# Kernel tuning notes

Measured on AMD Instinct MI355X. Metric: run time of the kernel, lower is better.

## Reference

```python
import jax, jax.numpy as jnp
import numpy as np


def _rot_mat(thetas, scales):
    # thetas, scales: [bs, g] -> [bs, g, 9, 9] bilinear-interpolation matrices
    bs, g = thetas.shape
    t = thetas.reshape(-1)
    s = scales.reshape(-1)
    x = jnp.cos(t) * s
    y = jnp.sin(t) * s
    yp = -y
    z = jnp.zeros_like(x)
    o = jnp.ones_like(x)
    a = x - y; b = x * y; c = x + y; d = a * c; e = a + c
    ap = x - yp; bp = x * yp; cp = x + yp; dp = ap * cp; ep = ap + cp

    def M(rows):
        # rows: 9 lists of 9 [N]-arrays -> [9, 9, N]
        return jnp.stack([jnp.stack(r, axis=0) for r in rows], axis=0)

    ctr = [z, z, z, z, o, z, z, z, z]

    pb1 = M([
        [a, 1 - a, z, z, z, z, z, z, z],
        [z, 1 - y, y, z, z, z, z, z, z],
        [z, z, a, z, z, 1 - a, z, z, z],
        [y, z, z, 1 - y, z, z, z, z, z],
        ctr,
        [z, z, z, z, z, 1 - y, z, z, y],
        [z, z, z, 1 - a, z, z, a, z, z],
        [z, z, z, z, z, z, y, 1 - y, z],
        [z, z, z, z, z, z, z, 1 - a, a]])
    pb2 = M([
        [a, 1 - a, z, z, z, z, z, z, z],
        [z, x - b, b, z, 1 - c + b, y - b, z, z, z],
        [z, z, a, z, z, 1 - a, z, z, z],
        [b, y - b, z, x - b, 1 - c + b, z, z, z, z],
        ctr,
        [z, z, z, z, 1 - c + b, x - b, z, y - b, b],
        [z, z, z, 1 - a, z, z, a, z, z],
        [z, z, z, y - b, 1 - c + b, z, b, x - b, z],
        [z, z, z, z, z, z, z, 1 - a, a]])
    ps1 = M([
        [d, a - d, z, c - d, 1 - e + d, z, z, z, z],
        [z, x - b, b, z, 1 - c + b, y - b, z, z, z],
        [z, c - d, d, z, 1 - e + d, a - d, z, z, z],
        [b, y - b, z, x - b, 1 - c + b, z, z, z, z],
        ctr,
        [z, z, z, z, 1 - c + b, x - b, z, y - b, b],
        [z, z, z, a - d, 1 - e + d, z, d, c - d, z],
        [z, z, z, y - b, 1 - c + b, z, b, x - b, z],
        [z, z, z, z, 1 - e + d, c - d, z, a - d, d]])
    ps2 = pb2  # identical in the source
    nb1 = M([
        [cp, z, z, 1 - cp, z, z, z, z, z],
        [yp, 1 - yp, z, z, z, z, z, z, z],
        [z, 1 - cp, cp, z, z, z, z, z, z],
        [z, z, z, 1 - yp, z, z, yp, z, z],
        ctr,
        [z, z, yp, z, z, 1 - yp, z, z, z],
        [z, z, z, z, z, z, cp, 1 - cp, z],
        [z, z, z, z, z, z, z, 1 - yp, yp],
        [z, z, z, z, z, 1 - cp, z, z, cp]])
    nb2 = M([
        [cp, z, z, 1 - cp, z, z, z, z, z],
        [bp, x - bp, z, yp - bp, 1 - cp + bp, z, z, z, z],
        [z, 1 - cp, cp, z, z, z, z, z, z],
        [z, z, z, x - bp, 1 - cp + bp, z, bp, yp - bp, z],
        ctr,
        [z, yp - bp, bp, z, 1 - cp + bp, x - bp, z, z, z],
        [z, z, z, z, z, z, cp, 1 - cp, z],
        [z, z, z, z, 1 - cp + bp, yp - bp, z, x - bp, bp],
        [z, z, z, z, z, 1 - cp, z, z, cp]])
    ns1 = M([
        [dp, cp - dp, z, ap - dp, 1 - ep + dp, z, z, z, z],
        [bp, x - bp, z, yp - bp, 1 - cp + bp, z, z, z, z],
        [z, ap - dp, dp, z, 1 - ep + dp, cp - dp, z, z, z],
        [z, yp - bp, bp, z, 1 - cp + bp, x - bp, z, z, z],
        ctr,
        [z, z, z, x - bp, 1 - cp + bp, z, bp, yp - bp, z],
        [z, z, z, cp - dp, 1 - ep + dp, z, dp, ap - dp, z],
        [z, z, z, z, 1 - cp + bp, yp - bp, z, x - bp, bp],
        [z, z, z, z, 1 - ep + dp, ap - dp, z, cp - dp, dp]])
    ns2 = nb2  # mirrors the positive branch where small_2 == big_2

    m_pos = (t >= 0.0)[None, None, :]
    m_big = (s >= 1.0)[None, None, :]
    m_1 = (jnp.abs(t) <= jnp.pi / 4)[None, None, :]
    pos = jnp.where(m_big, jnp.where(m_1, pb1, pb2), jnp.where(m_1, ps1, ps2))
    neg = jnp.where(m_big, jnp.where(m_1, nb1, nb2), jnp.where(m_1, ns1, ns2))
    rot = jnp.where(m_pos, pos, neg)  # [9, 9, bs*g]
    return jnp.transpose(rot, (2, 0, 1)).reshape(bs, g, 9, 9)


def _forward(x, thetas, scales, lambdas, weight):
    # x: [B, Cin, H, W]; weight: [n, Cout, Cin, 3, 3]; thetas/scales/lambdas: [B, n]
    B, Cin, H, W = x.shape
    n, Cout = weight.shape[0], weight.shape[1]
    rot = _rot_mat(thetas, scales) * lambdas[:, :, None, None]  # [B, n, 9, 9]
    w9 = weight.reshape(n, Cout, Cin, 9)
    # per-sample transformed kernel: sum over kernel_number n and source taps j
    w = jnp.einsum('bnij,nocj->bioc', rot, w9)  # [B, 9, Cout, Cin]
    w = jnp.transpose(w, (0, 2, 3, 1)).reshape(B * Cout, Cin, 3, 3)
    xg = x.reshape(1, B * Cin, H, W)
    out = jax.lax.conv_general_dilated(
        xg, w, window_strides=(1, 1), padding=((1, 1), (1, 1)),
        dimension_numbers=('NCHW', 'OIHW', 'NCHW'), feature_group_count=B)
    return out.reshape(B, Cout, H, W)


def setup_inputs() -> dict:
    key = jax.random.key(0)
    ks = jax.random.split(key, 5)
    B, Cin, Cout, H, W, n = 16, 256, 256, 64, 64, 4
    x = jax.random.normal(ks[0], (B, Cin, H, W), dtype=jnp.float32)
    thetas = jax.random.uniform(ks[1], (B, n), minval=-1.2, maxval=1.2, dtype=jnp.float32)
    scales = jax.random.uniform(ks[2], (B, n), minval=0.5, maxval=1.5, dtype=jnp.float32)
    lambdas = jax.nn.softmax(jax.random.normal(ks[3], (B, n), dtype=jnp.float32), axis=-1)
    weight = jax.random.normal(ks[4], (n, Cout, Cin, 3, 3), dtype=jnp.float32) * 0.05
    return {"x": x, "thetas": thetas, "scales": scales, "lambdas": lambdas, "weight": weight}


def reference(x, thetas, scales, lambdas, weight):
    return _forward(x, thetas, scales, lambdas, weight)
```

## Files before the change

### kernel.cpp

```cpp
#include <hip/hip_runtime.h>
#include <cstdint>
#include <cstddef>

typedef unsigned short ushort_t;
typedef __attribute__((ext_vector_type(4))) float f32x4;
typedef __attribute__((ext_vector_type(8))) short s16x8;

#define PI_4F 0.78539816339744830962f

__device__ inline ushort_t f2bf(float f) {
  unsigned int u = __float_as_uint(f);
  u = u + 0x7fffu + ((u >> 16) & 1u);
  return (ushort_t)(u >> 16);
}

__global__ void rot_kernel(const float* __restrict__ thetas, const float* __restrict__ scales,
                           const float* __restrict__ lambdas, float* __restrict__ rot) {
  int tid = threadIdx.x;
  float t = thetas[tid], s = scales[tid], lam = lambdas[tid];
  float xv = cosf(t) * s, yv = sinf(t) * s;
  bool pos = (t >= 0.0f), big = (s >= 1.0f), m1 = (fabsf(t) <= PI_4F);
  float M[81];
#pragma unroll
  for (int i = 0; i < 81; ++i) M[i] = 0.0f;
  M[36 + 4] = 1.0f;
  if (pos) {
    float a = xv - yv, bb = xv * yv, c = xv + yv;
    if (m1 && big) {
      M[0] = a; M[1] = 1 - a;
      M[9 + 1] = 1 - yv; M[9 + 2] = yv;
      M[18 + 2] = a; M[18 + 5] = 1 - a;
      M[27 + 0] = yv; M[27 + 3] = 1 - yv;
      M[45 + 5] = 1 - yv; M[45 + 8] = yv;
      M[54 + 3] = 1 - a; M[54 + 6] = a;
      M[63 + 6] = yv; M[63 + 7] = 1 - yv;
      M[72 + 7] = 1 - a; M[72 + 8] = a;
    } else if (m1) {
      float d = a * c, e = a + c;
      M[0] = d; M[1] = a - d; M[3] = c - d; M[4] = 1 - e + d;
      M[9 + 1] = xv - bb; M[9 + 2] = bb; M[9 + 4] = 1 - c + bb; M[9 + 5] = yv - bb;
      M[18 + 1] = c - d; M[18 + 2] = d; M[18 + 4] = 1 - e + d; M[18 + 5] = a - d;
      M[27 + 0] = bb; M[27 + 1] = yv - bb; M[27 + 3] = xv - bb; M[27 + 4] = 1 - c + bb;
      M[45 + 4] = 1 - c + bb; M[45 + 5] = xv - bb; M[45 + 7] = yv - bb; M[45 + 8] = bb;
      M[54 + 3] = a - d; M[54 + 4] = 1 - e + d; M[54 + 6] = d; M[54 + 7] = c - d;
      M[63 + 3] = yv - bb; M[63 + 4] = 1 - c + bb; M[63 + 6] = bb; M[63 + 7] = xv - bb;
      M[72 + 4] = 1 - e + d; M[72 + 5] = c - d; M[72 + 7] = a - d; M[72 + 8] = d;
    } else {
      M[0] = a; M[1] = 1 - a;
      M[9 + 1] = xv - bb; M[9 + 2] = bb; M[9 + 4] = 1 - c + bb; M[9 + 5] = yv - bb;
      M[18 + 2] = a; M[18 + 5] = 1 - a;
      M[27 + 0] = bb; M[27 + 1] = yv - bb; M[27 + 3] = xv - bb; M[27 + 4] = 1 - c + bb;
      M[45 + 4] = 1 - c + bb; M[45 + 5] = xv - bb; M[45 + 7] = yv - bb; M[45 + 8] = bb;
      M[54 + 3] = 1 - a; M[54 + 6] = a;
      M[63 + 3] = yv - bb; M[63 + 4] = 1 - c + bb; M[63 + 6] = bb; M[63 + 7] = xv - bb;
      M[72 + 7] = 1 - a; M[72 + 8] = a;
    }
  } else {
    float yp = -yv;
    float ap = xv - yp, bp = xv * yp, cp = xv + yp;
    if (m1 && big) {
      M[0] = cp; M[3] = 1 - cp;
      M[9 + 0] = yp; M[9 + 1] = 1 - yp;
      M[18 + 1] = 1 - cp; M[18 + 2] = cp;
      M[27 + 3] = 1 - yp; M[27 + 6] = yp;
      M[45 + 2] = yp; M[45 + 5] = 1 - yp;
      M[54 + 6] = cp; M[54 + 7] = 1 - cp;
      M[63 + 7] = 1 - yp; M[63 + 8] = yp;
      M[72 + 5] = 1 - cp; M[72 + 8] = cp;
    } else if (m1) {
      float dp = ap * cp, ep = ap + cp;
      M[0] = dp; M[1] = cp - dp; M[3] = ap - dp; M[4] = 1 - ep + dp;
      M[9 + 0] = bp; M[9 + 1] = xv - bp; M[9 + 3] = yp - bp; M[9 + 4] = 1 - cp + bp;
      M[18 + 1] = ap - dp; M[18 + 2] = dp; M[18 + 4] = 1 - ep + dp; M[18 + 5] = cp - dp;
      M[27 + 1] = yp - bp; M[27 + 2] = bp; M[27 + 4] = 1 - cp + bp; M[27 + 5] = xv - bp;
      M[45 + 3] = xv - bp; M[45 + 4] = 1 - cp + bp; M[45 + 6] = bp; M[45 + 7] = yp - bp;
      M[54 + 3] = cp - dp; M[54 + 4] = 1 - ep + dp; M[54 + 6] = dp; M[54 + 7] = ap - dp;
      M[63 + 4] = 1 - cp + bp; M[63 + 5] = yp - bp; M[63 + 7] = xv - bp; M[63 + 8] = bp;
      M[72 + 4] = 1 - ep + dp; M[72 + 5] = ap - dp; M[72 + 7] = cp - dp; M[72 + 8] = dp;
    } else {
      M[0] = cp; M[3] = 1 - cp;
      M[9 + 0] = bp; M[9 + 1] = xv - bp; M[9 + 3] = yp - bp; M[9 + 4] = 1 - cp + bp;
      M[18 + 1] = 1 - cp; M[18 + 2] = cp;
      M[27 + 3] = xv - bp; M[27 + 4] = 1 - cp + bp; M[27 + 6] = bp; M[27 + 7] = yp - bp;
      M[45 + 1] = yp - bp; M[45 + 2] = bp; M[45 + 4] = 1 - cp + bp; M[45 + 5] = xv - bp;
      M[54 + 6] = cp; M[54 + 7] = 1 - cp;
      M[63 + 4] = 1 - cp + bp; M[63 + 5] = yp - bp; M[63 + 7] = xv - bp; M[63 + 8] = bp;
      M[72 + 5] = 1 - cp; M[72 + 8] = cp;
    }
  }
  float* r = rot + tid * 81;
#pragma unroll
  for (int i = 0; i < 81; ++i) r[i] = M[i] * lam;
}

__global__ void wt_kernel(const float* __restrict__ weight, const float* __restrict__ rot,
                          ushort_t* __restrict__ wtout) {
  const int o = blockIdx.x, bg = blockIdx.y;
  const int c = threadIdx.x;
  float wv[4][9];
#pragma unroll
  for (int n = 0; n < 4; ++n) {
    const float* wp = weight + (((size_t)(n * 256 + o)) * 256 + c) * 9;
#pragma unroll
    for (int j = 0; j < 9; ++j) wv[n][j] = wp[j];
  }
#pragma unroll
  for (int bl = 0; bl < 4; ++bl) {
    const int b = bg * 4 + bl;
#pragma unroll
    for (int i = 0; i < 9; ++i) {
      float acc = 0.0f;
#pragma unroll
      for (int n = 0; n < 4; ++n) {
        const float* r = rot + (b * 4 + n) * 81 + i * 9;
#pragma unroll
        for (int j = 0; j < 9; ++j) acc = fmaf(r[j], wv[n][j], acc);
      }
      wtout[((size_t)((b * 9 + i) * 256 + o)) * 256 + c] = f2bf(acc);
    }
  }
}

__global__ void border_zero(ushort_t* __restrict__ xpad) {
  const int p = blockIdx.x, b = blockIdx.y;
  int h, w;
  if (p < 66) { h = 0; w = p; }
  else if (p < 132) { h = 65; w = p - 66; }
  else if (p < 196) { w = 0; h = p - 131; }
  else { w = 65; h = p - 195; }
  size_t base = ((size_t)(b * 4356 + h * 66 + w)) * 256 + threadIdx.x * 4;
  *(uint2*)(xpad + base) = make_uint2(0u, 0u);
}

__global__ void transpose_kernel(const float* __restrict__ x, ushort_t* __restrict__ xpad) {
  __shared__ ushort_t tile[64][65];
  const int b = blockIdx.z, ct = blockIdx.y, st = blockIdx.x;
  const int t = threadIdx.x;
  const int l = t & 63, wv = t >> 6;
  const int c0 = ct * 64;
  const float* xb = x + ((size_t)(b * 256 + c0)) * 4096 + st * 64;
#pragma unroll
  for (int k = 0; k < 16; ++k) {
    int c_l = wv + 4 * k;
    tile[l][c_l] = f2bf(xb[(size_t)c_l * 4096 + l]);
  }
  __syncthreads();
  const int hw_l0 = t >> 4, c4 = (t & 15) * 4;
#pragma unroll
  for (int k = 0; k < 4; ++k) {
    int w = hw_l0 + 16 * k;
    uint2 v = *(const uint2*)&tile[w][c4];
    *(uint2*)&xpad[((size_t)(b * 4356 + (st + 1) * 66 + (w + 1))) * 256 + c0 + c4] = v;
  }
}

__device__ inline void gload16(const ushort_t* g, ushort_t* l) {
  __builtin_amdgcn_global_load_lds(
      (const __attribute__((address_space(1))) unsigned int*)g,
      (__attribute__((address_space(3))) unsigned int*)l, 16, 0, 0);
}

#define WAITB(N)                                                      \
  asm volatile("s_waitcnt vmcnt(" #N ") lgkmcnt(0)\n\ts_barrier" ::: "memory")

__global__ __launch_bounds__(512, 4) void conv_kernel(
    const ushort_t* __restrict__ xpad, const ushort_t* __restrict__ wt,
    float* __restrict__ out) {
  __shared__ __align__(16) ushort_t As0[8192], As1[8192], As2[8192];
  __shared__ __align__(16) ushort_t Bs0[4096], Bs1[4096], Bs2[4096];

  const int id = blockIdx.x;
  const int xcd = id & 7;
  const int jj = id >> 3;
  const int b = xcd * 2 + (jj >> 5);
  const int ntile = jj & 31;

  const int t = threadIdx.x;
  const int wave = t >> 6, lane = t & 63;
  const int wm = wave & 3, wn = wave >> 2;
  const int lr = lane & 15, lq = lane >> 4;
  const int h0 = ntile * 2;

  const ushort_t* wt_b = wt + (size_t)b * 589824;
  const ushort_t* xp_b = xpad + (size_t)b * 1115136;

  const int lrow = t >> 2;
  const int cg8 = (((t & 3) ^ ((t >> 3) & 3)) * 8);
  const int rsw = (lr >> 1) & 3;
  const int aoff = (wm * 64 + lr) * 32 + ((lq ^ rsw) * 8);
  const int boff = (wn * 64 + lr) * 32 + ((lq ^ rsw) * 8);
  const int nrow2 = 2 * (lrow >> 6);

  f32x4 acc[4][4];
#pragma unroll
  for (int i = 0; i < 4; ++i)
#pragma unroll
    for (int j2 = 0; j2 < 4; ++j2) acc[i][j2] = (f32x4)(0.0f);

  auto stage = [&](int ks, ushort_t* Ad, ushort_t* Bd) {
    const int tap = ks >> 3;
    const int c0k = (ks & 7) << 5;
    const int kh = tap / 3, kw = tap - kh * 3;
    const ushort_t* ga = wt_b + ((size_t)(tap * 256 + lrow)) * 256 + c0k + cg8;
    gload16(ga, Ad + wave * 512);
    gload16(ga + 128 * 256, Ad + 4096 + wave * 512);
    const int sp = (h0 + kh) * 66 + kw + lrow + nrow2;
    gload16(xp_b + (size_t)sp * 256 + c0k + cg8, Bd + wave * 512);
  };

  auto compute = [&](const ushort_t* Ab, const ushort_t* Bb) {
    s16x8 bfr[4];
#pragma unroll
    for (int ni = 0; ni < 4; ++ni)
      bfr[ni] = *(const s16x8*)(Bb + boff + ni * 512);
#pragma unroll
    for (int mi = 0; mi < 4; ++mi) {
      s16x8 af = *(const s16x8*)(Ab + aoff + mi * 512);
#pragma unroll
      for (int ni = 0; ni < 4; ++ni)
        acc[mi][ni] = __builtin_amdgcn_mfma_f32_16x16x32_bf16(af, bfr[ni], acc[mi][ni], 0, 0, 0);
    }
  };

  stage(0, As0, Bs0);
  stage(1, As1, Bs1);

#pragma unroll 1
  for (int kk = 0; kk < 23; ++kk) {
    const int ks = kk * 3;
    WAITB(3);
    stage(ks + 2, As2, Bs2);
    compute(As0, Bs0);
    WAITB(3);
    stage(ks + 3, As0, Bs0);
    compute(As1, Bs1);
    WAITB(3);
    stage(ks + 4, As1, Bs1);
    compute(As2, Bs2);
  }
  WAITB(3);
  stage(71, As2, Bs2);
  compute(As0, Bs0);
  WAITB(3);
  compute(As1, Bs1);
  WAITB(0);
  compute(As2, Bs2);

  float* ob = out + ((size_t)(b * 256 + wm * 64)) * 4096 + ntile * 128 + wn * 64 + lr;
#pragma unroll
  for (int mi = 0; mi < 4; ++mi)
#pragma unroll
    for (int r = 0; r < 4; ++r) {
      float* orow = ob + (size_t)(mi * 16 + lq * 4 + r) * 4096;
#pragma unroll
      for (int ni = 0; ni < 4; ++ni) orow[ni * 16] = acc[mi][ni][r];
    }
}

extern "C" void kernel_launch(void* const* d_in, const int* in_sizes, int n_in,
                              void* d_out, int out_size, void* d_ws, size_t ws_size,
                              hipStream_t stream) {
  const float* x = (const float*)d_in[0];
  const float* thetas = (const float*)d_in[1];
  const float* scales = (const float*)d_in[2];
  const float* lambdas = (const float*)d_in[3];
  const float* weight = (const float*)d_in[4];
  float* out = (float*)d_out;

  float* rot_ws = (float*)d_ws;
  ushort_t* wt_ws = (ushort_t*)((char*)d_ws + 32768);
  ushort_t* xpad_ws = (ushort_t*)((char*)d_ws + 32768 + 18874368);

  rot_kernel<<<1, 64, 0, stream>>>(thetas, scales, lambdas, rot_ws);
  wt_kernel<<<dim3(256, 4), 256, 0, stream>>>(weight, rot_ws, wt_ws);
  border_zero<<<dim3(260, 16), 64, 0, stream>>>(xpad_ws);
  transpose_kernel<<<dim3(64, 4, 16), 256, 0, stream>>>(x, xpad_ws);
  conv_kernel<<<512, 512, 0, stream>>>(xpad_ws, wt_ws, out);
}
```

Before: 227.7 us.

## Fuse border zeroing into transpose, vectorize prep kernels, raise MFMA priority

Drops the separate border_zero launch and has the transpose kernel zero the padded borders itself. The transpose now reads float4 vectors with a padded LDS tile. The weight kernel computes two channels per thread and stores packed bf16 pairs. s_setprio is raised around the MFMA block in the conv kernel. Together these aim to cut launch overhead and memory-access inefficiency in the preprocessing kernels, at the risk of LDS bank conflicts from the new tile write pattern.

```diff
diff --git a/kernel.cpp b/kernel.cpp
--- a/kernel.cpp
+++ b/kernel.cpp
@@ -93,64 +93,78 @@
   for (int i = 0; i < 81; ++i) r[i] = M[i] * lam;
 }
 
-__global__ void wt_kernel(const float* __restrict__ weight, const float* __restrict__ rot,
-                          ushort_t* __restrict__ wtout) {
+__global__ __launch_bounds__(128) void wt_kernel(const float* __restrict__ weight,
+                                                 const float* __restrict__ rot,
+                                                 ushort_t* __restrict__ wtout) {
   const int o = blockIdx.x, bg = blockIdx.y;
-  const int c = threadIdx.x;
-  float wv[4][9];
+  const int cid = threadIdx.x;
+  const int c = cid * 2;
+  float wv0[4][9], wv1[4][9];
 #pragma unroll
   for (int n = 0; n < 4; ++n) {
     const float* wp = weight + (((size_t)(n * 256 + o)) * 256 + c) * 9;
 #pragma unroll
-    for (int j = 0; j < 9; ++j) wv[n][j] = wp[j];
+    for (int j = 0; j < 9; ++j) { wv0[n][j] = wp[j]; wv1[n][j] = wp[9 + j]; }
   }
 #pragma unroll
   for (int bl = 0; bl < 4; ++bl) {
     const int b = bg * 4 + bl;
 #pragma unroll
     for (int i = 0; i < 9; ++i) {
-      float acc = 0.0f;
+      float a0 = 0.0f, a1 = 0.0f;
 #pragma unroll
       for (int n = 0; n < 4; ++n) {
         const float* r = rot + (b * 4 + n) * 81 + i * 9;
 #pragma unroll
-        for (int j = 0; j < 9; ++j) acc = fmaf(r[j], wv[n][j], acc);
+        for (int j = 0; j < 9; ++j) {
+          a0 = fmaf(r[j], wv0[n][j], a0);
+          a1 = fmaf(r[j], wv1[n][j], a1);
+        }
       }
-      wtout[((size_t)((b * 9 + i) * 256 + o)) * 256 + c] = f2bf(acc);
-    }
-  }
-}
-
-__global__ void border_zero(ushort_t* __restrict__ xpad) {
-  const int p = blockIdx.x, b = blockIdx.y;
-  int h, w;
-  if (p < 66) { h = 0; w = p; }
-  else if (p < 132) { h = 65; w = p - 66; }
-  else if (p < 196) { w = 0; h = p - 131; }
-  else { w = 65; h = p - 195; }
-  size_t base = ((size_t)(b * 4356 + h * 66 + w)) * 256 + threadIdx.x * 4;
-  *(uint2*)(xpad + base) = make_uint2(0u, 0u);
-}
-
-__global__ void transpose_kernel(const float* __restrict__ x, ushort_t* __restrict__ xpad) {
-  __shared__ ushort_t tile[64][65];
+      unsigned int word = (unsigned int)f2bf(a0) | ((unsigned int)f2bf(a1) << 16);
+      *(unsigned int*)&wtout[((size_t)((b * 9 + i) * 256 + o)) * 256 + c] = word;
+    }
+  }
+}
+
+__global__ __launch_bounds__(256) void transpose_kernel(const float* __restrict__ x,
+                                                        ushort_t* __restrict__ xpad) {
+  __shared__ ushort_t tile[64][68];
   const int b = blockIdx.z, ct = blockIdx.y, st = blockIdx.x;
   const int t = threadIdx.x;
-  const int l = t & 63, wv = t >> 6;
   const int c0 = ct * 64;
   const float* xb = x + ((size_t)(b * 256 + c0)) * 4096 + st * 64;
 #pragma unroll
-  for (int k = 0; k < 16; ++k) {
-    int c_l = wv + 4 * k;
-    tile[l][c_l] = f2bf(xb[(size_t)c_l * 4096 + l]);
+  for (int k = 0; k < 4; ++k) {
+    int idx = t + 256 * k;
+    int c_l = idx >> 4, w4 = (idx & 15) * 4;
+    float4 v = *(const float4*)&xb[(size_t)c_l * 4096 + w4];
+    tile[w4 + 0][c_l] = f2bf(v.x);
+    tile[w4 + 1][c_l] = f2bf(v.y);
+    tile[w4 + 2][c_l] = f2bf(v.z);
+    tile[w4 + 3][c_l] = f2bf(v.w);
   }
   __syncthreads();
-  const int hw_l0 = t >> 4, c4 = (t & 15) * 4;
+  const int c4 = (t & 15) * 4, wl = t >> 4;
+  const size_t rowbase = (size_t)(b * 4356 + (st + 1) * 66) * 256 + c0;
 #pragma unroll
   for (int k = 0; k < 4; ++k) {
-    int w = hw_l0 + 16 * k;
+    int w = wl + 16 * k;
     uint2 v = *(const uint2*)&tile[w][c4];
-    *(uint2*)&xpad[((size_t)(b * 4356 + (st + 1) * 66 + (w + 1))) * 256 + c0 + c4] = v;
+    *(uint2*)&xpad[rowbase + (size_t)(w + 1) * 256 + c4] = v;
+  }
+  if (t < 32) {
+    int w = (t & 16) ? 65 : 0;
+    int cc = (t & 15) * 4;
+    *(uint2*)&xpad[rowbase + (size_t)w * 256 + cc] = make_uint2(0u, 0u);
+  }
+  if (st == 0 || st == 63) {
+    const int h = (st == 0) ? 0 : 65;
+    const size_t hb = (size_t)(b * 4356 + h * 66) * 256 + c0;
+    for (int idx = t; idx < 66 * 16; idx += 256) {
+      int w = idx >> 4, cc = (idx & 15) * 4;
+      *(uint2*)&xpad[hb + (size_t)w * 256 + cc] = make_uint2(0u, 0u);
+    }
   }
 }
 
@@ -213,6 +227,7 @@
 #pragma unroll
     for (int ni = 0; ni < 4; ++ni)
       bfr[ni] = *(const s16x8*)(Bb + boff + ni * 512);
+    __builtin_amdgcn_s_setprio(1);
 #pragma unroll
     for (int mi = 0; mi < 4; ++mi) {
       s16x8 af = *(const s16x8*)(Ab + aoff + mi * 512);
@@ -220,6 +235,7 @@
       for (int ni = 0; ni < 4; ++ni)
         acc[mi][ni] = __builtin_amdgcn_mfma_f32_16x16x32_bf16(af, bfr[ni], acc[mi][ni], 0, 0, 0);
     }
+    __builtin_amdgcn_s_setprio(0);
   };
 
   stage(0, As0, Bs0);
@@ -272,8 +288,7 @@
   ushort_t* xpad_ws = (ushort_t*)((char*)d_ws + 32768 + 18874368);
 
   rot_kernel<<<1, 64, 0, stream>>>(thetas, scales, lambdas, rot_ws);
-  wt_kernel<<<dim3(256, 4), 256, 0, stream>>>(weight, rot_ws, wt_ws);
-  border_zero<<<dim3(260, 16), 64, 0, stream>>>(xpad_ws);
+  wt_kernel<<<dim3(256, 4), 128, 0, stream>>>(weight, rot_ws, wt_ws);
   transpose_kernel<<<dim3(64, 4, 16), 256, 0, stream>>>(x, xpad_ws);
   conv_kernel<<<512, 512, 0, stream>>>(xpad_ws, wt_ws, out);
 }
```

Measured after the change: 235.2 us. 1.03x slower.
